# Optimization experiments

Hardware: AMD Instinct MI355X
Metric: run time of the kernel (lower is better)

## Reference

```python
import jax, jax.numpy as jnp
import numpy as np

NUM_NODES = 10101   # 1 root + 100 supers + 10000 leaves
NUM_LEAVES = 10000
TEMPERATURE = 1.0
# weights from the source: root_weight=0, super_weight=1, leaf_weight=1
PATH_WEIGHTS = np.array([0.0, 1.0, 1.0], dtype=np.float32)
TOTAL_WEIGHT = float(PATH_WEIGHTS.sum())


def setup_inputs() -> dict:
    key = jax.random.key(0)
    k1, k2 = jax.random.split(key)
    features = jax.random.normal(k1, (8192, 128), dtype=jnp.float32)
    prototypes = jax.random.normal(k2, (NUM_NODES, 128), dtype=jnp.float32)
    # hierarchy: leaf i (node id 101+i) -> path [root=0, super=1+i//100, leaf=101+i]
    leaf = np.arange(NUM_LEAVES)
    path_idx = np.stack([np.zeros(NUM_LEAVES, dtype=np.int32),
                         (1 + leaf // 100).astype(np.int32),
                         (101 + leaf).astype(np.int32)], axis=1)  # [L, 3]
    return {"features": features, "prototypes": prototypes,
            "path_idx": jnp.asarray(path_idx)}


def reference(features, prototypes, path_idx):
    # ProCoLoss stand-in: node-level logits [N, num_nodes]
    node_logits = jnp.einsum('nd,cd->nc', features, prototypes) / TEMPERATURE
    # gather 3 path logits per leaf and weighted-sum (replaces per-leaf loop)
    gathered = node_logits[:, path_idx]                      # [N, L, 3]
    w = jnp.asarray(PATH_WEIGHTS)
    leaf_logits = jnp.einsum('nlk,k->nl', gathered, w) / TOTAL_WEIGHT  # [N, L]
    return leaf_logits
```

## Files before the change

### kernel.cpp

```cpp
#include <hip/hip_runtime.h>
#include <hip/hip_bf16.h>
#include <stdint.h>

#define M_DIM      8192
#define K_DIM      128
#define NUM_LEAVES 10000
#define N_PAD      10112
#define NT         79
#define MT         64
#define LDS_STRIDE 136
#define T_STRIDE   132

typedef __attribute__((ext_vector_type(8))) short bf16x8;
typedef __attribute__((ext_vector_type(4))) float f32x4;

static __device__ __forceinline__ unsigned short f2bf(float f) {
    union { float f; uint32_t u; } v; v.f = f;
    uint32_t u = v.u;
    u += 0x7FFFu + ((u >> 16) & 1u);
    return (unsigned short)(u >> 16);
}

__global__ void prep_features(const float* __restrict__ F, unsigned short* __restrict__ Fb) {
    int t = blockIdx.x * blockDim.x + threadIdx.x;
    float4 v = ((const float4*)F)[t];
    ushort4 o;
    o.x = f2bf(v.x); o.y = f2bf(v.y); o.z = f2bf(v.z); o.w = f2bf(v.w);
    ((ushort4*)Fb)[t] = o;
}

__global__ void prep_q(const float* __restrict__ P, const int* __restrict__ idx,
                       unsigned short* __restrict__ Qb) {
    int t = blockIdx.x * blockDim.x + threadIdx.x;
    int l = t >> 5;
    int c = (t & 31) << 2;
    ushort4 o;
    if (l < NUM_LEAVES) {
        int i1 = idx[l * 3 + 1];
        int i2 = idx[l * 3 + 2];
        float4 a = *(const float4*)&P[(size_t)i1 * K_DIM + c];
        float4 b = *(const float4*)&P[(size_t)i2 * K_DIM + c];
        o.x = f2bf(0.5f * (a.x + b.x));
        o.y = f2bf(0.5f * (a.y + b.y));
        o.z = f2bf(0.5f * (a.z + b.z));
        o.w = f2bf(0.5f * (a.w + b.w));
    } else {
        o.x = 0; o.y = 0; o.z = 0; o.w = 0;
    }
    *(ushort4*)&Qb[(size_t)l * K_DIM + c] = o;
}

__global__ __launch_bounds__(256, 2) void gemm_fq(
    const unsigned short* __restrict__ Fb,
    const unsigned short* __restrict__ Qb,
    float* __restrict__ out) {
    __shared__ __align__(16) unsigned char smem[2 * 128 * LDS_STRIDE * 2];
    unsigned short* As = (unsigned short*)smem;
    unsigned short* Bs = As + 128 * LDS_STRIDE;
    float* T = (float*)smem;

    const int bn = blockIdx.x;
    const int bm = blockIdx.y;
    const int tid = threadIdx.x;

    {
        const uint4* gA = (const uint4*)(Fb + (size_t)bm * 128 * K_DIM);
        const uint4* gB = (const uint4*)(Qb + (size_t)bn * 128 * K_DIM);
#pragma unroll
        for (int i = 0; i < 8; ++i) {
            int c = tid + i * 256;
            int r = c >> 4;
            int c8 = (c & 15) << 3;
            uint4 va = gA[c];
            uint4 vb = gB[c];
            *(uint4*)&As[r * LDS_STRIDE + c8] = va;
            *(uint4*)&Bs[r * LDS_STRIDE + c8] = vb;
        }
    }
    __syncthreads();

    const int lane = tid & 63;
    const int w    = tid >> 6;
    const int wm   = (w >> 1) * 64;
    const int wn   = (w & 1) * 64;
    const int l15  = lane & 15;
    const int quad = lane >> 4;

    f32x4 acc[4][4] = {};

#pragma unroll
    for (int kt = 0; kt < 4; ++kt) {
        const int k0 = kt * 32 + quad * 8;
        bf16x8 af[4], bfr[4];
#pragma unroll
        for (int i = 0; i < 4; ++i) {
            af[i]  = *(const bf16x8*)&As[(wm + i * 16 + l15) * LDS_STRIDE + k0];
            bfr[i] = *(const bf16x8*)&Bs[(wn + i * 16 + l15) * LDS_STRIDE + k0];
        }
#pragma unroll
        for (int mi = 0; mi < 4; ++mi)
#pragma unroll
            for (int ni = 0; ni < 4; ++ni)
                acc[mi][ni] = __builtin_amdgcn_mfma_f32_16x16x32_bf16(
                    bfr[ni], af[mi], acc[mi][ni], 0, 0, 0);
    }

    __syncthreads();

    {
        const int nbase = wm + l15;
        const int cb    = wn + quad * 4;
#pragma unroll
        for (int mi = 0; mi < 4; ++mi) {
            float* trow = T + (size_t)(nbase + mi * 16) * T_STRIDE;
#pragma unroll
            for (int ni = 0; ni < 4; ++ni) {
                *(f32x4*)&trow[cb + ni * 16] = acc[mi][ni];
            }
        }
    }
    __syncthreads();

    {
        const int half = lane >> 5;
        const int cx   = (lane & 31) << 2;
        int vcols = NUM_LEAVES - bn * 128;
        if (vcols > 128) vcols = 128;
        const bool ok = cx < vcols;
        float* gbase = out + (size_t)(bm * 128) * NUM_LEAVES + (size_t)bn * 128 + cx;
        const int r0 = w * 32 + half;
#pragma unroll
        for (int it = 0; it < 16; ++it) {
            const int r = r0 + it * 2;
            f32x4 v = *(const f32x4*)&T[(size_t)r * T_STRIDE + cx];
            if (ok) {
                __builtin_nontemporal_store(v, (f32x4*)(gbase + (size_t)r * NUM_LEAVES));
            }
        }
    }
}

extern "C" void kernel_launch(void* const* d_in, const int* in_sizes, int n_in,
                              void* d_out, int out_size, void* d_ws, size_t ws_size,
                              hipStream_t stream) {
    const float* F  = (const float*)d_in[0];
    const float* P  = (const float*)d_in[1];
    const int* idx  = (const int*)d_in[2];
    float* out      = (float*)d_out;

    unsigned short* Fb = (unsigned short*)d_ws;
    unsigned short* Qb = Fb + (size_t)M_DIM * K_DIM;

    prep_features<<<(M_DIM * K_DIM / 4) / 256, 256, 0, stream>>>(F, Fb);
    prep_q<<<(N_PAD * 32) / 256, 256, 0, stream>>>(P, idx, Qb);
    gemm_fq<<<dim3(NT, MT), 256, 0, stream>>>(Fb, Qb, out);
}
```

Measured before the change: 338.5 us.

## Halve GEMM LDS footprint by splitting K loads and epilogue into two phases

The kernel now loads the A and B tiles in two K-halves into a half-size LDS buffer. The output transpose is done in two 64-row phases so it reuses the smaller buffer. Launch bounds are raised from 2 to 4 blocks per CU to use the freed LDS for more concurrent blocks and more latency hiding on this store-bound kernel. In exchange each block has extra barriers and serialized load/compute phases, and register pressure may rise under the tighter launch bound.

```diff
diff --git a/kernel.cpp b/kernel.cpp
--- a/kernel.cpp
+++ b/kernel.cpp
@@ -8,7 +8,7 @@
 #define N_PAD      10112
 #define NT         79
 #define MT         64
-#define LDS_STRIDE 136
+#define HS         68
 #define T_STRIDE   132
 
 typedef __attribute__((ext_vector_type(8))) short bf16x8;
@@ -50,34 +50,18 @@
     *(ushort4*)&Qb[(size_t)l * K_DIM + c] = o;
 }
 
-__global__ __launch_bounds__(256, 2) void gemm_fq(
+__global__ __launch_bounds__(256, 4) void gemm_fq(
     const unsigned short* __restrict__ Fb,
     const unsigned short* __restrict__ Qb,
     float* __restrict__ out) {
-    __shared__ __align__(16) unsigned char smem[2 * 128 * LDS_STRIDE * 2];
-    unsigned short* As = (unsigned short*)smem;
-    unsigned short* Bs = As + 128 * LDS_STRIDE;
+    __shared__ __align__(16) unsigned char smem[2 * 128 * HS * 2];
+    unsigned short* As2 = (unsigned short*)smem;
+    unsigned short* Bs2 = As2 + 128 * HS;
     float* T = (float*)smem;
 
     const int bn = blockIdx.x;
     const int bm = blockIdx.y;
     const int tid = threadIdx.x;
-
-    {
-        const uint4* gA = (const uint4*)(Fb + (size_t)bm * 128 * K_DIM);
-        const uint4* gB = (const uint4*)(Qb + (size_t)bn * 128 * K_DIM);
-#pragma unroll
-        for (int i = 0; i < 8; ++i) {
-            int c = tid + i * 256;
-            int r = c >> 4;
-            int c8 = (c & 15) << 3;
-            uint4 va = gA[c];
-            uint4 vb = gB[c];
-            *(uint4*)&As[r * LDS_STRIDE + c8] = va;
-            *(uint4*)&Bs[r * LDS_STRIDE + c8] = vb;
-        }
-    }
-    __syncthreads();
 
     const int lane = tid & 63;
     const int w    = tid >> 6;
@@ -86,57 +70,76 @@
     const int l15  = lane & 15;
     const int quad = lane >> 4;
 
+    const uint4* gA = (const uint4*)(Fb + (size_t)bm * 128 * K_DIM);
+    const uint4* gB = (const uint4*)(Qb + (size_t)bn * 128 * K_DIM);
+
     f32x4 acc[4][4] = {};
 
 #pragma unroll
-    for (int kt = 0; kt < 4; ++kt) {
-        const int k0 = kt * 32 + quad * 8;
-        bf16x8 af[4], bfr[4];
+    for (int h = 0; h < 2; ++h) {
 #pragma unroll
         for (int i = 0; i < 4; ++i) {
-            af[i]  = *(const bf16x8*)&As[(wm + i * 16 + l15) * LDS_STRIDE + k0];
-            bfr[i] = *(const bf16x8*)&Bs[(wn + i * 16 + l15) * LDS_STRIDE + k0];
+            int c = tid + i * 256;
+            int r = c >> 3;
+            int q = c & 7;
+            uint4 va = gA[r * 16 + h * 8 + q];
+            uint4 vb = gB[r * 16 + h * 8 + q];
+            *(uint4*)&As2[r * HS + q * 8] = va;
+            *(uint4*)&Bs2[r * HS + q * 8] = vb;
         }
+        __syncthreads();
+
 #pragma unroll
-        for (int mi = 0; mi < 4; ++mi)
+        for (int kt = 0; kt < 2; ++kt) {
+            const int k0 = kt * 32 + quad * 8;
+            bf16x8 af[4], bfr[4];
 #pragma unroll
-            for (int ni = 0; ni < 4; ++ni)
-                acc[mi][ni] = __builtin_amdgcn_mfma_f32_16x16x32_bf16(
-                    bfr[ni], af[mi], acc[mi][ni], 0, 0, 0);
+            for (int i = 0; i < 4; ++i) {
+                af[i]  = *(const bf16x8*)&As2[(wm + i * 16 + l15) * HS + k0];
+                bfr[i] = *(const bf16x8*)&Bs2[(wn + i * 16 + l15) * HS + k0];
+            }
+#pragma unroll
+            for (int mi = 0; mi < 4; ++mi)
+#pragma unroll
+                for (int ni = 0; ni < 4; ++ni)
+                    acc[mi][ni] = __builtin_amdgcn_mfma_f32_16x16x32_bf16(
+                        bfr[ni], af[mi], acc[mi][ni], 0, 0, 0);
+        }
+        __syncthreads();
     }
 
-    __syncthreads();
+    int vcols = NUM_LEAVES - bn * 128;
+    if (vcols > 128) vcols = 128;
+    const int half = lane >> 5;
+    const int cx   = (lane & 31) << 2;
+    const bool ok  = cx < vcols;
+    float* gbase = out + (size_t)bn * 128 + cx;
 
-    {
-        const int nbase = wm + l15;
-        const int cb    = wn + quad * 4;
 #pragma unroll
-        for (int mi = 0; mi < 4; ++mi) {
-            float* trow = T + (size_t)(nbase + mi * 16) * T_STRIDE;
+    for (int ph = 0; ph < 2; ++ph) {
+        if ((w >> 1) == ph) {
+            const int cb = wn + quad * 4;
 #pragma unroll
-            for (int ni = 0; ni < 4; ++ni) {
-                *(f32x4*)&trow[cb + ni * 16] = acc[mi][ni];
+            for (int mi = 0; mi < 4; ++mi) {
+                float* trow = T + (size_t)(mi * 16 + l15) * T_STRIDE;
+#pragma unroll
+                for (int ni = 0; ni < 4; ++ni)
+                    *(f32x4*)&trow[cb + ni * 16] = acc[mi][ni];
             }
         }
-    }
-    __syncthreads();
+        __syncthreads();
 
-    {
-        const int half = lane >> 5;
-        const int cx   = (lane & 31) << 2;
-        int vcols = NUM_LEAVES - bn * 128;
-        if (vcols > 128) vcols = 128;
-        const bool ok = cx < vcols;
-        float* gbase = out + (size_t)(bm * 128) * NUM_LEAVES + (size_t)bn * 128 + cx;
-        const int r0 = w * 32 + half;
+        const int r0 = w * 16 + half;
 #pragma unroll
-        for (int it = 0; it < 16; ++it) {
+        for (int it = 0; it < 8; ++it) {
             const int r = r0 + it * 2;
             f32x4 v = *(const f32x4*)&T[(size_t)r * T_STRIDE + cx];
             if (ok) {
-                __builtin_nontemporal_store(v, (f32x4*)(gbase + (size_t)r * NUM_LEAVES));
+                const int grow = bm * 128 + ph * 64 + r;
+                __builtin_nontemporal_store(v, (f32x4*)(gbase + (size_t)grow * NUM_LEAVES));
             }
         }
+        if (ph == 0) __syncthreads();
     }
 }
 
```

New measurement: 376.7 us. 11.3% more time.

## Widen GEMM tile to 128x256 with 512 threads and two-phase LDS epilogue

Applied to the files above, without the earlier changes.

Each block now computes a 128x256 output tile with 8 waves instead of 128x128 with 4 waves, which halves the number of blocks and the redundant loads of the feature tile. The epilogue stages half the rows at a time through LDS and writes 1 KB contiguous row segments, so stores are wider. The cost is one block per CU, more LDS per block, extra barriers, and some wasted columns in the last tile (40*256 covers well past 10000).

```diff
diff --git a/kernel.cpp b/kernel.cpp
--- a/kernel.cpp
+++ b/kernel.cpp
@@ -6,10 +6,10 @@
 #define K_DIM      128
 #define NUM_LEAVES 10000
 #define N_PAD      10112
-#define NT         79
-#define MT         64
+#define NTB        40
+#define MTB        64
 #define LDS_STRIDE 136
-#define T_STRIDE   132
+#define T_STRIDE2  260
 
 typedef __attribute__((ext_vector_type(8))) short bf16x8;
 typedef __attribute__((ext_vector_type(4))) float f32x4;
@@ -50,11 +50,11 @@
     *(ushort4*)&Qb[(size_t)l * K_DIM + c] = o;
 }
 
-__global__ __launch_bounds__(256, 2) void gemm_fq(
+__global__ __launch_bounds__(512, 1) void gemm_fq(
     const unsigned short* __restrict__ Fb,
     const unsigned short* __restrict__ Qb,
     float* __restrict__ out) {
-    __shared__ __align__(16) unsigned char smem[2 * 128 * LDS_STRIDE * 2];
+    __shared__ __align__(16) unsigned char smem[(128 + 256) * LDS_STRIDE * 2];
     unsigned short* As = (unsigned short*)smem;
     unsigned short* Bs = As + 128 * LDS_STRIDE;
     float* T = (float*)smem;
@@ -65,24 +65,34 @@
 
     {
         const uint4* gA = (const uint4*)(Fb + (size_t)bm * 128 * K_DIM);
-        const uint4* gB = (const uint4*)(Qb + (size_t)bn * 128 * K_DIM);
+#pragma unroll
+        for (int i = 0; i < 4; ++i) {
+            int c = tid + i * 512;
+            int r = c >> 4;
+            int q = c & 15;
+            uint4 v = gA[c];
+            *(uint4*)&As[r * LDS_STRIDE + q * 8] = v;
+        }
+    }
+    {
+        const uint4* gQ = (const uint4*)Qb;
 #pragma unroll
         for (int i = 0; i < 8; ++i) {
-            int c = tid + i * 256;
+            int c = tid + i * 512;
             int r = c >> 4;
-            int c8 = (c & 15) << 3;
-            uint4 va = gA[c];
-            uint4 vb = gB[c];
-            *(uint4*)&As[r * LDS_STRIDE + c8] = va;
-            *(uint4*)&Bs[r * LDS_STRIDE + c8] = vb;
+            int q = c & 15;
+            int gr = bn * 256 + r;
+            uint4 v = make_uint4(0u, 0u, 0u, 0u);
+            if (gr < N_PAD) v = gQ[(size_t)gr * 16 + q];
+            *(uint4*)&Bs[r * LDS_STRIDE + q * 8] = v;
         }
     }
     __syncthreads();
 
     const int lane = tid & 63;
     const int w    = tid >> 6;
-    const int wm   = (w >> 1) * 64;
-    const int wn   = (w & 1) * 64;
+    const int wm   = (w >> 2) * 64;
+    const int wn   = (w & 3) * 64;
     const int l15  = lane & 15;
     const int quad = lane >> 4;
 
@@ -104,39 +114,37 @@
                 acc[mi][ni] = __builtin_amdgcn_mfma_f32_16x16x32_bf16(
                     bfr[ni], af[mi], acc[mi][ni], 0, 0, 0);
     }
-
     __syncthreads();
 
-    {
-        const int nbase = wm + l15;
-        const int cb    = wn + quad * 4;
+    const int cx   = lane << 2;
+    const int ccol = bn * 256 + cx;
+    const bool ok  = ccol < NUM_LEAVES;
+    float* gbase = out + ccol;
+
 #pragma unroll
-        for (int mi = 0; mi < 4; ++mi) {
-            float* trow = T + (size_t)(nbase + mi * 16) * T_STRIDE;
+    for (int ph = 0; ph < 2; ++ph) {
+        if ((w >> 2) == ph) {
+            const int cb = wn + quad * 4;
 #pragma unroll
-            for (int ni = 0; ni < 4; ++ni) {
-                *(f32x4*)&trow[cb + ni * 16] = acc[mi][ni];
+            for (int mi = 0; mi < 4; ++mi) {
+                float* trow = T + (size_t)(mi * 16 + l15) * T_STRIDE2;
+#pragma unroll
+                for (int ni = 0; ni < 4; ++ni)
+                    *(f32x4*)&trow[cb + ni * 16] = acc[mi][ni];
             }
         }
-    }
-    __syncthreads();
+        __syncthreads();
 
-    {
-        const int half = lane >> 5;
-        const int cx   = (lane & 31) << 2;
-        int vcols = NUM_LEAVES - bn * 128;
-        if (vcols > 128) vcols = 128;
-        const bool ok = cx < vcols;
-        float* gbase = out + (size_t)(bm * 128) * NUM_LEAVES + (size_t)bn * 128 + cx;
-        const int r0 = w * 32 + half;
 #pragma unroll
-        for (int it = 0; it < 16; ++it) {
-            const int r = r0 + it * 2;
-            f32x4 v = *(const f32x4*)&T[(size_t)r * T_STRIDE + cx];
+        for (int it = 0; it < 8; ++it) {
+            const int r = w * 8 + it;
+            f32x4 v = *(const f32x4*)&T[(size_t)r * T_STRIDE2 + cx];
             if (ok) {
-                __builtin_nontemporal_store(v, (f32x4*)(gbase + (size_t)r * NUM_LEAVES));
+                const int grow = bm * 128 + ph * 64 + r;
+                __builtin_nontemporal_store(v, (f32x4*)(gbase + (size_t)grow * NUM_LEAVES));
             }
         }
+        if (ph == 0) __syncthreads();
     }
 }
 
@@ -153,5 +161,5 @@
 
     prep_features<<<(M_DIM * K_DIM / 4) / 256, 256, 0, stream>>>(F, Fb);
     prep_q<<<(N_PAD * 32) / 256, 256, 0, stream>>>(P, idx, Qb);
-    gemm_fq<<<dim3(NT, MT), 256, 0, stream>>>(Fb, Qb, out);
+    gemm_fq<<<dim3(NTB, MTB), 512, 0, stream>>>(Fb, Qb, out);
 }
```

New measurement: 347.2 us. +2.6%, slower.
